# Kernel tuning notes

Measured on AMD Instinct MI355X. Metric: run time of the kernel, lower is better.

## Reference

```python
import jax, jax.numpy as jnp
import numpy as np
from jax import lax

B, S, H = 2, 1024, 1024   # batch, seq, hidden_size
I = 512                   # moe_intermediate_size
E = 16                    # num_experts
TOP_K = 8                 # num_experts_per_tok


def setup_inputs() -> dict:
    key = jax.random.key(0)
    ks = jax.random.split(key, 5)
    scale_h = 1.0 / np.sqrt(H)
    scale_i = 1.0 / np.sqrt(I)
    return {
        "hidden_states": jax.random.normal(ks[0], (B, S, H), dtype=jnp.float32),
        "gate_w": jax.random.normal(ks[1], (H, E), dtype=jnp.float32) * scale_h,   # router
        "w_gate": jax.random.normal(ks[2], (E, H, I), dtype=jnp.float32) * scale_h,
        "w_up":   jax.random.normal(ks[3], (E, H, I), dtype=jnp.float32) * scale_h,
        "w_down": jax.random.normal(ks[4], (E, I, H), dtype=jnp.float32) * scale_i,
    }


def reference(hidden_states, gate_w, w_gate, w_up, w_down):
    b, s, h = hidden_states.shape
    x = hidden_states.reshape(-1, h)                      # [T, H]
    T = x.shape[0]

    router_logits = x @ gate_w                            # [T, E]
    probs = jax.nn.softmax(router_logits.astype(jnp.float32), axis=-1)
    top_w, top_i = lax.top_k(probs, TOP_K)                # [T, K]
    top_w = top_w / jnp.sum(top_w, axis=-1, keepdims=True)  # norm_topk_prob
    top_w = top_w.astype(x.dtype)

    # Dense per-token combine weights [T, E]; zero for unselected experts
    combine = jnp.zeros((T, E), dtype=x.dtype)
    combine = combine.at[jnp.arange(T)[:, None], top_i].add(top_w)

    # Scan over experts: masked gated-MLP, weighted accumulate (exact math;
    # unselected tokens contribute with weight 0, matching index_add scatter).
    def expert_step(acc, ws):
        wg, wu, wd, ce = ws                               # ce: [T] combine weights
        hmid = jax.nn.silu(x @ wg) * (x @ wu)             # [T, I]
        return acc + (hmid @ wd) * ce[:, None], None

    out, _ = lax.scan(expert_step, jnp.zeros_like(x),
                      (w_gate, w_up, w_down, combine.T))
    return out.reshape(b, s, h), router_logits
```

## Files before the change

kernel.cpp:

```cpp
#include <hip/hip_runtime.h>

typedef __attribute__((ext_vector_type(8))) short bf16x8;
typedef __attribute__((ext_vector_type(4))) float f32x4;
typedef __attribute__((ext_vector_type(4))) unsigned short u16x4;


static __device__ __forceinline__ unsigned short f2bfu(float f) {
  union { float f; unsigned u; } v; v.f = f;
  return (unsigned short)((v.u + 0x7fffu + ((v.u >> 16) & 1u)) >> 16);
}

static __device__ __forceinline__ float bfu2f(unsigned short u) {
  union { unsigned u; float f; } v; v.u = ((unsigned)u) << 16; return v.f;
}

static __device__ __forceinline__ void gload_lds16(const void* g, void* l) {
  __builtin_amdgcn_global_load_lds(
      (const __attribute__((address_space(1))) unsigned int*)g,
      (__attribute__((address_space(3))) unsigned int*)l, 16, 0, 0);
}

__global__ __launch_bounds__(256) void k_prep(const float* __restrict__ wga,
                                              const float* __restrict__ wup,
                                              const float* __restrict__ wdo,
                                              unsigned short* __restrict__ wgt,
                                              unsigned short* __restrict__ wut,
                                              unsigned short* __restrict__ wdt2,
                                              const float* __restrict__ x,
                                              const float* __restrict__ gw,
                                              float* __restrict__ combine,
                                              float* __restrict__ logits,
                                              unsigned short* __restrict__ xb) {
  const int bid = blockIdx.x;
  if (bid < 6144) {
    __shared__ float tile[64][65];
    const int zz = bid >> 7;
    const int rem = bid & 127;
    const float* src;
    unsigned short* dst;
    int C, ostride, c0, r0;
    if (zz < 16)      { src = wga + (size_t)zz * 524288; dst = wgt + (size_t)zz * 524288; C = 512; ostride = 1024; c0 = (rem & 7) * 64; r0 = (rem >> 3) * 64; }
    else if (zz < 32) { src = wup + (size_t)(zz-16) * 524288; dst = wut + (size_t)(zz-16) * 524288; C = 512; ostride = 1024; c0 = (rem & 7) * 64; r0 = (rem >> 3) * 64; }
    else              { src = wdo + (size_t)(zz-32) * 524288; dst = wdt2 + (size_t)(zz-32) * 524288; C = 1024; ostride = 512; c0 = (rem & 15) * 64; r0 = (rem >> 4) * 64; }
    int cc = (threadIdx.x & 15) * 4, rr = threadIdx.x >> 4;
#pragma unroll
    for (int i = 0; i < 4; ++i) {
      float4 v = *(const float4*)(src + (size_t)(r0 + rr + i * 16) * C + c0 + cc);
      tile[rr + i * 16][cc + 0] = v.x; tile[rr + i * 16][cc + 1] = v.y;
      tile[rr + i * 16][cc + 2] = v.z; tile[rr + i * 16][cc + 3] = v.w;
    }
    __syncthreads();
#pragma unroll
    for (int i = 0; i < 4; ++i) {
      int oc = rr + i * 16;
      u16x4 o = { f2bfu(tile[cc + 0][oc]), f2bfu(tile[cc + 1][oc]),
                  f2bfu(tile[cc + 2][oc]), f2bfu(tile[cc + 3][oc]) };
      *(u16x4*)(dst + (size_t)(c0 + oc) * ostride + r0 + cc) = o;
    }
    return;
  }
  const int t = (bid - 6144) * 4 + (threadIdx.x >> 6);
  const int lane = threadIdx.x & 63;
  const float* xr = x + (size_t)t * 1024;
  unsigned short* xbr = xb + (size_t)t * 1024;
  float acc[16];
#pragma unroll
  for (int e = 0; e < 16; ++e) acc[e] = 0.f;
  for (int h = lane; h < 1024; h += 64) {
    float xv = xr[h];
    xbr[h] = f2bfu(xv);
    const float4* gr = (const float4*)(gw + (size_t)h * 16);
#pragma unroll
    for (int q = 0; q < 4; ++q) {
      float4 g4 = gr[q];
      acc[q * 4 + 0] += xv * g4.x;
      acc[q * 4 + 1] += xv * g4.y;
      acc[q * 4 + 2] += xv * g4.z;
      acc[q * 4 + 3] += xv * g4.w;
    }
  }
#pragma unroll
  for (int e = 0; e < 16; ++e) {
#pragma unroll
    for (int off = 32; off > 0; off >>= 1)
      acc[e] += __shfl_xor(acc[e], off);
  }
  if (lane < 16) logits[(size_t)t * 16 + lane] = acc[lane];

  float m = acc[0];
#pragma unroll
  for (int e = 1; e < 16; ++e) m = fmaxf(m, acc[e]);
  unsigned sel = 0u;
  for (int k = 0; k < 8; ++k) {
    float best = -3.4e38f; int bi = 0;
#pragma unroll
    for (int e = 0; e < 16; ++e)
      if (!((sel >> e) & 1u) && acc[e] > best) { best = acc[e]; bi = e; }
    sel |= 1u << bi;
  }
  float s = 0.f;
#pragma unroll
  for (int e = 0; e < 16; ++e)
    if ((sel >> e) & 1u) s += expf(acc[e] - m);
  float inv = 1.f / s;
  if (lane < 16)
    combine[(size_t)t * 16 + lane] = ((sel >> lane) & 1u) ? expf(acc[lane] - m) * inv : 0.f;
}

__global__ __launch_bounds__(256) void k_scan(const float* __restrict__ combine,
                                              unsigned short* __restrict__ idxlist,
                                              int* __restrict__ tokslot,
                                              int* __restrict__ counts) {
  __shared__ int wsum[4];
  const int e = blockIdx.x;
  const int tid = threadIdx.x;
  const int lane = tid & 63, w = tid >> 6;
  const int t0 = tid * 8;
  int flags = 0, cnt = 0;
#pragma unroll
  for (int j = 0; j < 8; ++j) {
    float c = combine[(size_t)(t0 + j) * 16 + e];
    if (c != 0.f) { flags |= 1 << j; ++cnt; }
  }
  int scan = cnt;
#pragma unroll
  for (int off = 1; off < 64; off <<= 1) {
    int v = __shfl_up(scan, off);
    if (lane >= off) scan += v;
  }
  if (lane == 63) wsum[w] = scan;
  __syncthreads();
  int base = 0;
  for (int i = 0; i < w; ++i) base += wsum[i];
  int pos = base + scan - cnt;
  for (int j = 0; j < 8; ++j) {
    if ((flags >> j) & 1) {
      idxlist[e * 2048 + pos] = (unsigned short)(t0 + j);
      tokslot[(t0 + j) * 16 + e] = pos;
      ++pos;
    } else {
      tokslot[(t0 + j) * 16 + e] = -1;
    }
  }
  if (tid == 255) counts[e] = base + scan;
}

__global__ __launch_bounds__(256) void k_gateup(const unsigned short* __restrict__ xb,
                                                const unsigned short* __restrict__ wgt,
                                                const unsigned short* __restrict__ wut,
                                                const unsigned short* __restrict__ idxlist,
                                                const int* __restrict__ counts,
                                                unsigned short* __restrict__ midp) {
  const int lb = (int)(blockIdx.x & 7) * 256 + (int)(blockIdx.x >> 3);
  const int p = lb & 255, it = lb >> 8;
  int e = -1, mt = 0, Ne = 0, gb = 0, acc = 0;
#pragma unroll
  for (int i = 0; i < 16; ++i) {
    int c = counts[i];
    int nt = (c + 127) >> 7;
    if (e < 0) {
      if (p < acc + nt) { e = i; mt = p - acc; Ne = c; }
      else gb += c;
    }
    acc += nt;
  }
  if (e < 0) return;
  const int m0 = mt * 128;
  const int i0 = it * 64;

  __shared__ alignas(16) char lds[49152];

  const int tid = threadIdx.x;
  const int lane = tid & 63;
  const int w = tid >> 6;
  const int wm = (w >> 1) * 64;
  const int wn = (w & 1) * 32;

  const int crow = lane >> 2;
  const int slog = (lane & 3) ^ ((crow >> 1) & 3);

  const unsigned short* wge = wgt + (size_t)e * (512 * 1024);
  const unsigned short* wue = wut + (size_t)e * (512 * 1024);

  const unsigned short* gsrc[4];
  int loff[4];
#pragma unroll
  for (int q = 0; q < 4; ++q) {
    int c = w * 4 + q;
    loff[q] = c * 1024;
    if (c < 8) {
      int slot = m0 + c * 16 + crow;
      slot = slot < Ne ? slot : Ne - 1;
      gsrc[q] = xb + (size_t)idxlist[e * 2048 + slot] * 1024 + slog * 8;
    } else if (c < 12) {
      gsrc[q] = wge + (size_t)(i0 + (c - 8) * 16 + crow) * 1024 + slog * 8;
    } else {
      gsrc[q] = wue + (size_t)(i0 + (c - 12) * 16 + crow) * 1024 + slog * 8;
    }
  }

  auto stage = [&](int buf, int k0) {
    char* base = lds + buf * 16384;
#pragma unroll
    for (int q = 0; q < 4; ++q)
      gload_lds16(gsrc[q] + k0, base + loff[q]);
  };

  const int r0 = lane & 15;
  const int gp16 = ((lane >> 4) ^ ((r0 >> 1) & 3)) << 4;
  const int aoff  = ((wm + r0) << 6) + gp16;
  const int bgoff = 8192  + ((wn + r0) << 6) + gp16;
  const int buoff = 12288 + ((wn + r0) << 6) + gp16;

  f32x4 accg[4][2], accu[4][2];
#pragma unroll
  for (int fm = 0; fm < 4; ++fm)
#pragma unroll
    for (int fn = 0; fn < 2; ++fn) {
      accg[fm][fn] = f32x4{0.f, 0.f, 0.f, 0.f};
      accu[fm][fn] = f32x4{0.f, 0.f, 0.f, 0.f};
    }

  stage(0, 0);
  stage(1, 32);
  int cur = 0;
  for (int t = 0; t < 32; ++t) {
    if (t == 31) asm volatile("s_waitcnt vmcnt(0)" ::: "memory");
    else         asm volatile("s_waitcnt vmcnt(4)" ::: "memory");
    __builtin_amdgcn_s_barrier();
    const char* base = lds + cur * 16384;
    bf16x8 a[4], bg[2], bu[2];
#pragma unroll
    for (int fm = 0; fm < 4; ++fm) a[fm] = *(const bf16x8*)(base + aoff + fm * 1024);
#pragma unroll
    for (int fn = 0; fn < 2; ++fn) {
      bg[fn] = *(const bf16x8*)(base + bgoff + fn * 1024);
      bu[fn] = *(const bf16x8*)(base + buoff + fn * 1024);
    }
    asm volatile("s_waitcnt lgkmcnt(0)" ::: "memory");
    __builtin_amdgcn_sched_barrier(0);
    if (t + 2 < 32) {
      int nb = cur + 2; if (nb >= 3) nb -= 3;
      stage(nb, (t + 2) * 32);
    }
    __builtin_amdgcn_s_setprio(1);
#pragma unroll
    for (int fm = 0; fm < 4; ++fm)
#pragma unroll
      for (int fn = 0; fn < 2; ++fn) {
        accg[fm][fn] = __builtin_amdgcn_mfma_f32_16x16x32_bf16(a[fm], bg[fn], accg[fm][fn], 0, 0, 0);
        accu[fm][fn] = __builtin_amdgcn_mfma_f32_16x16x32_bf16(a[fm], bu[fn], accu[fm][fn], 0, 0, 0);
      }
    __builtin_amdgcn_s_setprio(0);
    if (++cur == 3) cur = 0;
  }

  const int gq = lane >> 4;
#pragma unroll
  for (int fm = 0; fm < 4; ++fm) {
#pragma unroll
    for (int jj = 0; jj < 4; ++jj) {
      int slot = m0 + wm + fm * 16 + gq * 4 + jj;
      if (slot >= Ne) continue;
#pragma unroll
      for (int fn = 0; fn < 2; ++fn) {
        float gv = accg[fm][fn][jj];
        float uv = accu[fm][fn][jj];
        float mv = gv / (1.f + __expf(-gv)) * uv;
        midp[(size_t)(gb + slot) * 512 + i0 + wn + fn * 16 + r0] = f2bfu(mv);
      }
    }
  }
}

__global__ __launch_bounds__(512) void k_down(const unsigned short* __restrict__ midp,
                                              const unsigned short* __restrict__ wdt2,
                                              const int* __restrict__ counts,
                                              unsigned short* __restrict__ dpk) {
  const int lb = (int)(blockIdx.x & 7) * 256 + (int)(blockIdx.x >> 3);
  const int mt = lb & 7, ht = (lb >> 3) & 15, e = lb >> 7;
  int Ne = counts[e], gb = 0;
#pragma unroll
  for (int i = 0; i < 16; ++i) { int c = counts[i]; if (i < e) gb += c; }
  const int m0 = mt * 256;
  if (m0 >= Ne) return;
  const int h0 = ht * 64;

  __shared__ alignas(16) char lds[61440];

  const int tid = threadIdx.x;
  const int lane = tid & 63;
  const int w = tid >> 6;
  const int wm = (w >> 1) * 64;
  const int wn = (w & 1) * 32;

  const int crow = lane >> 2;
  const int slog = (lane & 3) ^ ((crow >> 1) & 3);

  const unsigned short* bsrc = wdt2 + (size_t)e * (512 * 1024);

  const unsigned short* gsrcA[2];
  int loffA[2];
#pragma unroll
  for (int q = 0; q < 2; ++q) {
    int c = q * 8 + w;
    loffA[q] = c * 1024;
    int slot = m0 + c * 16 + crow;
    slot = slot < Ne ? slot : Ne - 1;
    gsrcA[q] = midp + (size_t)(gb + slot) * 512 + slog * 8;
  }
  const unsigned short* gsrcB = nullptr;
  int loffB = 0;
  if (w >= 4) {
    loffB = 16384 + (w - 4) * 1024;
    gsrcB = bsrc + (size_t)(h0 + (w - 4) * 16 + crow) * 512 + slog * 8;
  }

  auto stage = [&](int buf, int k0) {
    char* base = lds + buf * 20480;
#pragma unroll
    for (int q = 0; q < 2; ++q)
      gload_lds16(gsrcA[q] + k0, base + loffA[q]);
    if (gsrcB) gload_lds16(gsrcB + k0, base + loffB);
  };

  const int r0 = lane & 15;
  const int gp16 = ((lane >> 4) ^ ((r0 >> 1) & 3)) << 4;
  const int aoff = ((wm + r0) << 6) + gp16;
  const int boff = 16384 + ((wn + r0) << 6) + gp16;

  f32x4 acc[4][2];
#pragma unroll
  for (int fm = 0; fm < 4; ++fm)
#pragma unroll
    for (int fn = 0; fn < 2; ++fn) acc[fm][fn] = f32x4{0.f, 0.f, 0.f, 0.f};

  stage(0, 0);
  stage(1, 32);
  int cur = 0;
  for (int t = 0; t < 16; ++t) {
    if (t == 15)       asm volatile("s_waitcnt vmcnt(0)" ::: "memory");
    else if (w >= 4)   asm volatile("s_waitcnt vmcnt(3)" ::: "memory");
    else               asm volatile("s_waitcnt vmcnt(2)" ::: "memory");
    __builtin_amdgcn_s_barrier();
    const char* base = lds + cur * 20480;
    bf16x8 a[4], b[2];
#pragma unroll
    for (int fm = 0; fm < 4; ++fm) a[fm] = *(const bf16x8*)(base + aoff + fm * 1024);
#pragma unroll
    for (int fn = 0; fn < 2; ++fn) b[fn] = *(const bf16x8*)(base + boff + fn * 1024);
    asm volatile("s_waitcnt lgkmcnt(0)" ::: "memory");
    __builtin_amdgcn_sched_barrier(0);
    if (t + 2 < 16) {
      int nb = cur + 2; if (nb >= 3) nb -= 3;
      stage(nb, (t + 2) * 32);
    }
    __builtin_amdgcn_s_setprio(1);
#pragma unroll
    for (int fm = 0; fm < 4; ++fm)
#pragma unroll
      for (int fn = 0; fn < 2; ++fn)
        acc[fm][fn] = __builtin_amdgcn_mfma_f32_16x16x32_bf16(a[fm], b[fn], acc[fm][fn], 0, 0, 0);
    __builtin_amdgcn_s_setprio(0);
    if (++cur == 3) cur = 0;
  }

  const int gq = lane >> 4;
#pragma unroll
  for (int fm = 0; fm < 4; ++fm)
#pragma unroll
    for (int jj = 0; jj < 4; ++jj) {
      int slot = m0 + wm + fm * 16 + gq * 4 + jj;
      if (slot >= Ne) continue;
#pragma unroll
      for (int fn = 0; fn < 2; ++fn)
        dpk[(size_t)(gb + slot) * 1024 + h0 + wn + fn * 16 + r0] = f2bfu(acc[fm][fn][jj]);
    }
}

__global__ __launch_bounds__(128) void k_combine(const unsigned short* __restrict__ dpk,
                                                 const int* __restrict__ tokslot,
                                                 const int* __restrict__ counts,
                                                 const float* __restrict__ combine,
                                                 float* __restrict__ out) {
  __shared__ int gsl[16];
  __shared__ float cws[16];
  const int t = blockIdx.x;
  const int tid = threadIdx.x;
  if (tid < 16) {
    int eb = 0;
    for (int i = 0; i < tid; ++i) eb += counts[i];
    int sl = tokslot[t * 16 + tid];
    gsl[tid] = (sl >= 0) ? eb + sl : -1;
    cws[tid] = combine[(size_t)t * 16 + tid];
  }
  __syncthreads();
  float av[8];
#pragma unroll
  for (int j = 0; j < 8; ++j) av[j] = 0.f;
#pragma unroll
  for (int e = 0; e < 16; ++e) {
    int g = gsl[e];
    if (g < 0) continue;
    float cw = cws[e];
    bf16x8 v = *(const bf16x8*)(dpk + (size_t)g * 1024 + tid * 8);
#pragma unroll
    for (int j = 0; j < 8; ++j) av[j] += cw * bfu2f((unsigned short)v[j]);
  }
  float4 lo = { av[0], av[1], av[2], av[3] };
  float4 hi = { av[4], av[5], av[6], av[7] };
  float4* op = (float4*)(out + (size_t)t * 1024 + tid * 8);
  op[0] = lo;
  op[1] = hi;
}

extern "C" void kernel_launch(void* const* d_in, const int* in_sizes, int n_in,
                              void* d_out, int out_size, void* d_ws, size_t ws_size,
                              hipStream_t stream) {
  const float* x   = (const float*)d_in[0];
  const float* gw  = (const float*)d_in[1];
  const float* wga = (const float*)d_in[2];
  const float* wup = (const float*)d_in[3];
  const float* wdo = (const float*)d_in[4];
  float* out = (float*)d_out;
  float* logits = out + (size_t)2048 * 1024;

  char* ws = (char*)d_ws;
  unsigned short* xb   = (unsigned short*)(ws + 0);
  unsigned short* wgt  = (unsigned short*)(ws + 4194304);
  unsigned short* wut  = (unsigned short*)(ws + 20971520);
  unsigned short* wdt2 = (unsigned short*)(ws + 37748736);
  unsigned short* midp = (unsigned short*)(ws + 54525952);
  float* combine       = (float*)(ws + 71303168);
  int* tokslot         = (int*)(ws + 71434240);
  unsigned short* idxl = (unsigned short*)(ws + 71565312);
  int* counts          = (int*)(ws + 71630848);
  unsigned short* dpk  = (unsigned short*)(ws + 4194304);

  k_prep<<<6656, 256, 0, stream>>>(wga, wup, wdo, wgt, wut, wdt2, x, gw, combine, logits, xb);
  k_scan<<<16, 256, 0, stream>>>(combine, idxl, tokslot, counts);
  k_gateup<<<2048, 256, 0, stream>>>(xb, wgt, wut, idxl, counts, midp);
  k_down<<<2048, 512, 0, stream>>>(midp, wdt2, counts, dpk);
  k_combine<<<2048, 128, 0, stream>>>(dpk, tokslot, counts, combine, out);
}
```

Before: 143.9 us.

## Fuse gate/up weight fp32-to-bf16 conversion into gateup GEMM loader

Drops the separate transpose-and-convert pass for the gate and up weights in the prep kernel. The gateup kernel now reads the fp32 weights straight from global memory into registers, converts them to bf16, and writes them into LDS. This pipelines the work one stage ahead using double-buffered register arrays and adds a 3-blocks-per-CU launch bound. It removes a 64MB read and 32MB write pass. In exchange each gateup block re-reads fp32 weights, which costs more register pressure and more global traffic across the M tiles.

```diff
diff --git a/kernel.cpp b/kernel.cpp
--- a/kernel.cpp
+++ b/kernel.cpp
@@ -20,11 +20,7 @@
       (__attribute__((address_space(3))) unsigned int*)l, 16, 0, 0);
 }
 
-__global__ __launch_bounds__(256) void k_prep(const float* __restrict__ wga,
-                                              const float* __restrict__ wup,
-                                              const float* __restrict__ wdo,
-                                              unsigned short* __restrict__ wgt,
-                                              unsigned short* __restrict__ wut,
+__global__ __launch_bounds__(256) void k_prep(const float* __restrict__ wdo,
                                               unsigned short* __restrict__ wdt2,
                                               const float* __restrict__ x,
                                               const float* __restrict__ gw,
@@ -32,20 +28,17 @@
                                               float* __restrict__ logits,
                                               unsigned short* __restrict__ xb) {
   const int bid = blockIdx.x;
-  if (bid < 6144) {
+  if (bid < 2048) {
     __shared__ float tile[64][65];
     const int zz = bid >> 7;
     const int rem = bid & 127;
-    const float* src;
-    unsigned short* dst;
-    int C, ostride, c0, r0;
-    if (zz < 16)      { src = wga + (size_t)zz * 524288; dst = wgt + (size_t)zz * 524288; C = 512; ostride = 1024; c0 = (rem & 7) * 64; r0 = (rem >> 3) * 64; }
-    else if (zz < 32) { src = wup + (size_t)(zz-16) * 524288; dst = wut + (size_t)(zz-16) * 524288; C = 512; ostride = 1024; c0 = (rem & 7) * 64; r0 = (rem >> 3) * 64; }
-    else              { src = wdo + (size_t)(zz-32) * 524288; dst = wdt2 + (size_t)(zz-32) * 524288; C = 1024; ostride = 512; c0 = (rem & 15) * 64; r0 = (rem >> 4) * 64; }
+    const float* src = wdo + (size_t)zz * 524288;
+    unsigned short* dst = wdt2 + (size_t)zz * 524288;
+    const int c0 = (rem & 15) * 64, r0 = (rem >> 4) * 64;
     int cc = (threadIdx.x & 15) * 4, rr = threadIdx.x >> 4;
 #pragma unroll
     for (int i = 0; i < 4; ++i) {
-      float4 v = *(const float4*)(src + (size_t)(r0 + rr + i * 16) * C + c0 + cc);
+      float4 v = *(const float4*)(src + (size_t)(r0 + rr + i * 16) * 1024 + c0 + cc);
       tile[rr + i * 16][cc + 0] = v.x; tile[rr + i * 16][cc + 1] = v.y;
       tile[rr + i * 16][cc + 2] = v.z; tile[rr + i * 16][cc + 3] = v.w;
     }
@@ -55,11 +48,11 @@
       int oc = rr + i * 16;
       u16x4 o = { f2bfu(tile[cc + 0][oc]), f2bfu(tile[cc + 1][oc]),
                   f2bfu(tile[cc + 2][oc]), f2bfu(tile[cc + 3][oc]) };
-      *(u16x4*)(dst + (size_t)(c0 + oc) * ostride + r0 + cc) = o;
+      *(u16x4*)(dst + (size_t)(c0 + oc) * 512 + r0 + cc) = o;
     }
     return;
   }
-  const int t = (bid - 6144) * 4 + (threadIdx.x >> 6);
+  const int t = (bid - 2048) * 4 + (threadIdx.x >> 6);
   const int lane = threadIdx.x & 63;
   const float* xr = x + (size_t)t * 1024;
   unsigned short* xbr = xb + (size_t)t * 1024;
@@ -145,12 +138,12 @@
   if (tid == 255) counts[e] = base + scan;
 }
 
-__global__ __launch_bounds__(256) void k_gateup(const unsigned short* __restrict__ xb,
-                                                const unsigned short* __restrict__ wgt,
-                                                const unsigned short* __restrict__ wut,
-                                                const unsigned short* __restrict__ idxlist,
-                                                const int* __restrict__ counts,
-                                                unsigned short* __restrict__ midp) {
+__global__ __launch_bounds__(256, 3) void k_gateup(const unsigned short* __restrict__ xb,
+                                                   const float* __restrict__ wga,
+                                                   const float* __restrict__ wup,
+                                                   const unsigned short* __restrict__ idxlist,
+                                                   const int* __restrict__ counts,
+                                                   unsigned short* __restrict__ midp) {
   const int lb = (int)(blockIdx.x & 7) * 256 + (int)(blockIdx.x >> 3);
   const int p = lb & 255, it = lb >> 8;
   int e = -1, mt = 0, Ne = 0, gb = 0, acc = 0;
@@ -179,31 +172,50 @@
   const int crow = lane >> 2;
   const int slog = (lane & 3) ^ ((crow >> 1) & 3);
 
-  const unsigned short* wge = wgt + (size_t)e * (512 * 1024);
-  const unsigned short* wue = wut + (size_t)e * (512 * 1024);
-
-  const unsigned short* gsrc[4];
-  int loff[4];
-#pragma unroll
-  for (int q = 0; q < 4; ++q) {
-    int c = w * 4 + q;
-    loff[q] = c * 1024;
-    if (c < 8) {
-      int slot = m0 + c * 16 + crow;
-      slot = slot < Ne ? slot : Ne - 1;
-      gsrc[q] = xb + (size_t)idxlist[e * 2048 + slot] * 1024 + slog * 8;
-    } else if (c < 12) {
-      gsrc[q] = wge + (size_t)(i0 + (c - 8) * 16 + crow) * 1024 + slog * 8;
-    } else {
-      gsrc[q] = wue + (size_t)(i0 + (c - 12) * 16 + crow) * 1024 + slog * 8;
-    }
-  }
-
-  auto stage = [&](int buf, int k0) {
+  const float* wge = wga + (size_t)e * 524288;
+  const float* wue = wup + (size_t)e * 524288;
+
+  const unsigned short* gsrcA[2];
+  int loffA[2];
+#pragma unroll
+  for (int q = 0; q < 2; ++q) {
+    int c = w * 2 + q;
+    loffA[q] = c * 1024;
+    int slot = m0 + c * 16 + crow;
+    slot = slot < Ne ? slot : Ne - 1;
+    gsrcA[q] = xb + (size_t)idxlist[e * 2048 + slot] * 1024 + slog * 8;
+  }
+  auto stageA = [&](int buf, int k0) {
     char* base = lds + buf * 16384;
 #pragma unroll
-    for (int q = 0; q < 4; ++q)
-      gload_lds16(gsrc[q] + k0, base + loff[q]);
+    for (int q = 0; q < 2; ++q)
+      gload_lds16(gsrcA[q] + k0, base + loffA[q]);
+  };
+
+  const int iloc = lane;
+  const float* gB = wge + (size_t)(w * 8) * 512 + i0 + iloc;
+  const float* uB = wue + (size_t)(w * 8) * 512 + i0 + iloc;
+  const int bwo = iloc * 64 + ((w ^ ((iloc >> 1) & 3)) << 4);
+
+  auto loadB = [&](float* bv, int T) {
+    const float* g = gB + (size_t)T * 32 * 512;
+    const float* u = uB + (size_t)T * 32 * 512;
+#pragma unroll
+    for (int j = 0; j < 8; ++j) {
+      bv[j] = g[(size_t)j * 512];
+      bv[8 + j] = u[(size_t)j * 512];
+    }
+  };
+  auto cvtwrite = [&](const float* bv, int buf) {
+    bf16x8 pg, pu;
+#pragma unroll
+    for (int j = 0; j < 8; ++j) {
+      pg[j] = (short)f2bfu(bv[j]);
+      pu[j] = (short)f2bfu(bv[8 + j]);
+    }
+    char* base = lds + buf * 16384;
+    *(bf16x8*)(base + 8192 + bwo) = pg;
+    *(bf16x8*)(base + 12288 + bwo) = pu;
   };
 
   const int r0 = lane & 15;
@@ -221,12 +233,17 @@
       accu[fm][fn] = f32x4{0.f, 0.f, 0.f, 0.f};
     }
 
-  stage(0, 0);
-  stage(1, 32);
+  float bvA[16], bvB[16];
+  stageA(0, 0);
+  stageA(1, 32);
+  loadB(bvA, 0);
+  cvtwrite(bvA, 0);
+  loadB(bvB, 1);
+
   int cur = 0;
-  for (int t = 0; t < 32; ++t) {
-    if (t == 31) asm volatile("s_waitcnt vmcnt(0)" ::: "memory");
-    else         asm volatile("s_waitcnt vmcnt(4)" ::: "memory");
+  auto body = [&](int t, float* bvLoad, float* bvCvt) {
+    if (t == 31) asm volatile("s_waitcnt vmcnt(0) lgkmcnt(0)" ::: "memory");
+    else         asm volatile("s_waitcnt vmcnt(18) lgkmcnt(0)" ::: "memory");
     __builtin_amdgcn_s_barrier();
     const char* base = lds + cur * 16384;
     bf16x8 a[4], bg[2], bu[2];
@@ -239,10 +256,13 @@
     }
     asm volatile("s_waitcnt lgkmcnt(0)" ::: "memory");
     __builtin_amdgcn_sched_barrier(0);
+    int nb1 = cur + 1; if (nb1 >= 3) nb1 -= 3;
+    int nb2 = cur + 2; if (nb2 >= 3) nb2 -= 3;
     if (t + 2 < 32) {
-      int nb = cur + 2; if (nb >= 3) nb -= 3;
-      stage(nb, (t + 2) * 32);
-    }
+      loadB(bvLoad, t + 2);
+      stageA(nb2, (t + 2) * 32);
+    }
+    if (t + 1 < 32) cvtwrite(bvCvt, nb1);
     __builtin_amdgcn_s_setprio(1);
 #pragma unroll
     for (int fm = 0; fm < 4; ++fm)
@@ -252,7 +272,12 @@
         accu[fm][fn] = __builtin_amdgcn_mfma_f32_16x16x32_bf16(a[fm], bu[fn], accu[fm][fn], 0, 0, 0);
       }
     __builtin_amdgcn_s_setprio(0);
-    if (++cur == 3) cur = 0;
+    cur = nb1;
+  };
+
+  for (int tt = 0; tt < 16; ++tt) {
+    body(2 * tt, bvA, bvB);
+    body(2 * tt + 1, bvB, bvA);
   }
 
   const int gq = lane >> 4;
@@ -427,19 +452,17 @@
 
   char* ws = (char*)d_ws;
   unsigned short* xb   = (unsigned short*)(ws + 0);
-  unsigned short* wgt  = (unsigned short*)(ws + 4194304);
-  unsigned short* wut  = (unsigned short*)(ws + 20971520);
-  unsigned short* wdt2 = (unsigned short*)(ws + 37748736);
-  unsigned short* midp = (unsigned short*)(ws + 54525952);
+  unsigned short* wdt2 = (unsigned short*)(ws + 4194304);
+  unsigned short* midp = (unsigned short*)(ws + 20971520);
+  unsigned short* dpk  = (unsigned short*)(ws + 37748736);
   float* combine       = (float*)(ws + 71303168);
   int* tokslot         = (int*)(ws + 71434240);
   unsigned short* idxl = (unsigned short*)(ws + 71565312);
   int* counts          = (int*)(ws + 71630848);
-  unsigned short* dpk  = (unsigned short*)(ws + 4194304);
-
-  k_prep<<<6656, 256, 0, stream>>>(wga, wup, wdo, wgt, wut, wdt2, x, gw, combine, logits, xb);
+
+  k_prep<<<2560, 256, 0, stream>>>(wdo, wdt2, x, gw, combine, logits, xb);
   k_scan<<<16, 256, 0, stream>>>(combine, idxl, tokslot, counts);
-  k_gateup<<<2048, 256, 0, stream>>>(xb, wgt, wut, idxl, counts, midp);
+  k_gateup<<<2048, 256, 0, stream>>>(xb, wga, wup, idxl, counts, midp);
   k_down<<<2048, 512, 0, stream>>>(midp, wdt2, counts, dpk);
   k_combine<<<2048, 128, 0, stream>>>(dpk, tokslot, counts, combine, out);
 }
```

After: 145.3 us. Within noise of the previous version (+1.0%).

## Make gate-up and down expert GEMMs persistent with atomic tile scheduling

Applied to the files above, without the earlier changes.

Converts k_gateup and k_down into persistent kernels with smaller fixed grids. Each block repeatedly grabs a work index from a global atomic counter, which k_scan resets, until all valid expert tiles are done. This removes launching many blocks that only exit because their expert has few tokens, balances uneven expert loads dynamically, and orders tiles so consecutive indices share the same token tile. It also adds occupancy hints to the launch bounds. The cost is an atomic plus a block barrier per tile, and a fixed grid size that may not fill the GPU evenly.

```diff
diff --git a/kernel.cpp b/kernel.cpp
--- a/kernel.cpp
+++ b/kernel.cpp
@@ -110,10 +110,12 @@
 __global__ __launch_bounds__(256) void k_scan(const float* __restrict__ combine,
                                               unsigned short* __restrict__ idxlist,
                                               int* __restrict__ tokslot,
-                                              int* __restrict__ counts) {
+                                              int* __restrict__ counts,
+                                              int* __restrict__ ctrs) {
   __shared__ int wsum[4];
   const int e = blockIdx.x;
   const int tid = threadIdx.x;
+  if (e == 0 && tid < 2) ctrs[tid] = 0;
   const int lane = tid & 63, w = tid >> 6;
   const int t0 = tid * 8;
   int flags = 0, cnt = 0;
@@ -145,30 +147,15 @@
   if (tid == 255) counts[e] = base + scan;
 }
 
-__global__ __launch_bounds__(256) void k_gateup(const unsigned short* __restrict__ xb,
-                                                const unsigned short* __restrict__ wgt,
-                                                const unsigned short* __restrict__ wut,
-                                                const unsigned short* __restrict__ idxlist,
-                                                const int* __restrict__ counts,
-                                                unsigned short* __restrict__ midp) {
-  const int lb = (int)(blockIdx.x & 7) * 256 + (int)(blockIdx.x >> 3);
-  const int p = lb & 255, it = lb >> 8;
-  int e = -1, mt = 0, Ne = 0, gb = 0, acc = 0;
-#pragma unroll
-  for (int i = 0; i < 16; ++i) {
-    int c = counts[i];
-    int nt = (c + 127) >> 7;
-    if (e < 0) {
-      if (p < acc + nt) { e = i; mt = p - acc; Ne = c; }
-      else gb += c;
-    }
-    acc += nt;
-  }
-  if (e < 0) return;
-  const int m0 = mt * 128;
-  const int i0 = it * 64;
-
+__global__ __launch_bounds__(256, 3) void k_gateup(const unsigned short* __restrict__ xb,
+                                                   const unsigned short* __restrict__ wgt,
+                                                   const unsigned short* __restrict__ wut,
+                                                   const unsigned short* __restrict__ idxlist,
+                                                   const int* __restrict__ counts,
+                                                   int* __restrict__ ctr,
+                                                   unsigned short* __restrict__ midp) {
   __shared__ alignas(16) char lds[49152];
+  __shared__ int sidx;
 
   const int tid = threadIdx.x;
   const int lane = tid & 63;
@@ -179,114 +166,136 @@
   const int crow = lane >> 2;
   const int slog = (lane & 3) ^ ((crow >> 1) & 3);
 
-  const unsigned short* wge = wgt + (size_t)e * (512 * 1024);
-  const unsigned short* wue = wut + (size_t)e * (512 * 1024);
-
-  const unsigned short* gsrc[4];
-  int loff[4];
-#pragma unroll
-  for (int q = 0; q < 4; ++q) {
-    int c = w * 4 + q;
-    loff[q] = c * 1024;
-    if (c < 8) {
-      int slot = m0 + c * 16 + crow;
-      slot = slot < Ne ? slot : Ne - 1;
-      gsrc[q] = xb + (size_t)idxlist[e * 2048 + slot] * 1024 + slog * 8;
-    } else if (c < 12) {
-      gsrc[q] = wge + (size_t)(i0 + (c - 8) * 16 + crow) * 1024 + slog * 8;
-    } else {
-      gsrc[q] = wue + (size_t)(i0 + (c - 12) * 16 + crow) * 1024 + slog * 8;
-    }
-  }
-
-  auto stage = [&](int buf, int k0) {
-    char* base = lds + buf * 16384;
-#pragma unroll
-    for (int q = 0; q < 4; ++q)
-      gload_lds16(gsrc[q] + k0, base + loff[q]);
-  };
-
   const int r0 = lane & 15;
   const int gp16 = ((lane >> 4) ^ ((r0 >> 1) & 3)) << 4;
   const int aoff  = ((wm + r0) << 6) + gp16;
   const int bgoff = 8192  + ((wn + r0) << 6) + gp16;
   const int buoff = 12288 + ((wn + r0) << 6) + gp16;
-
-  f32x4 accg[4][2], accu[4][2];
-#pragma unroll
-  for (int fm = 0; fm < 4; ++fm)
-#pragma unroll
-    for (int fn = 0; fn < 2; ++fn) {
-      accg[fm][fn] = f32x4{0.f, 0.f, 0.f, 0.f};
-      accu[fm][fn] = f32x4{0.f, 0.f, 0.f, 0.f};
-    }
-
-  stage(0, 0);
-  stage(1, 32);
-  int cur = 0;
-  for (int t = 0; t < 32; ++t) {
-    if (t == 31) asm volatile("s_waitcnt vmcnt(0)" ::: "memory");
-    else         asm volatile("s_waitcnt vmcnt(4)" ::: "memory");
-    __builtin_amdgcn_s_barrier();
-    const char* base = lds + cur * 16384;
-    bf16x8 a[4], bg[2], bu[2];
-#pragma unroll
-    for (int fm = 0; fm < 4; ++fm) a[fm] = *(const bf16x8*)(base + aoff + fm * 1024);
-#pragma unroll
-    for (int fn = 0; fn < 2; ++fn) {
-      bg[fn] = *(const bf16x8*)(base + bgoff + fn * 1024);
-      bu[fn] = *(const bf16x8*)(base + buoff + fn * 1024);
-    }
-    asm volatile("s_waitcnt lgkmcnt(0)" ::: "memory");
-    __builtin_amdgcn_sched_barrier(0);
-    if (t + 2 < 32) {
-      int nb = cur + 2; if (nb >= 3) nb -= 3;
-      stage(nb, (t + 2) * 32);
-    }
-    __builtin_amdgcn_s_setprio(1);
+  const int gq = lane >> 4;
+
+  int cl[16];
+#pragma unroll
+  for (int i = 0; i < 16; ++i) cl[i] = counts[i];
+  int pM = 0;
+#pragma unroll
+  for (int i = 0; i < 16; ++i) pM += (cl[i] + 127) >> 7;
+  const int total = pM * 8;
+
+  while (true) {
+    if (tid == 0) sidx = atomicAdd(ctr, 1);
+    __syncthreads();
+    const int idx = sidx;
+    if (idx >= total) return;
+    const int p = idx >> 3, it = idx & 7;
+    int e = -1, mt = 0, Ne = 0, gb = 0, acc = 0;
+#pragma unroll
+    for (int i = 0; i < 16; ++i) {
+      int c = cl[i];
+      int nt = (c + 127) >> 7;
+      if (e < 0) {
+        if (p < acc + nt) { e = i; mt = p - acc; Ne = c; }
+        else gb += c;
+      }
+      acc += nt;
+    }
+    const int m0 = mt * 128;
+    const int i0 = it * 64;
+
+    const unsigned short* wge = wgt + (size_t)e * (512 * 1024);
+    const unsigned short* wue = wut + (size_t)e * (512 * 1024);
+
+    const unsigned short* gsrc[4];
+    int loff[4];
+#pragma unroll
+    for (int q = 0; q < 4; ++q) {
+      int c = w * 4 + q;
+      loff[q] = c * 1024;
+      if (c < 8) {
+        int slot = m0 + c * 16 + crow;
+        slot = slot < Ne ? slot : Ne - 1;
+        gsrc[q] = xb + (size_t)idxlist[e * 2048 + slot] * 1024 + slog * 8;
+      } else if (c < 12) {
+        gsrc[q] = wge + (size_t)(i0 + (c - 8) * 16 + crow) * 1024 + slog * 8;
+      } else {
+        gsrc[q] = wue + (size_t)(i0 + (c - 12) * 16 + crow) * 1024 + slog * 8;
+      }
+    }
+
+    auto stage = [&](int buf, int k0) {
+      char* base = lds + buf * 16384;
+#pragma unroll
+      for (int q = 0; q < 4; ++q)
+        gload_lds16(gsrc[q] + k0, base + loff[q]);
+    };
+
+    f32x4 accg[4][2], accu[4][2];
 #pragma unroll
     for (int fm = 0; fm < 4; ++fm)
 #pragma unroll
       for (int fn = 0; fn < 2; ++fn) {
-        accg[fm][fn] = __builtin_amdgcn_mfma_f32_16x16x32_bf16(a[fm], bg[fn], accg[fm][fn], 0, 0, 0);
-        accu[fm][fn] = __builtin_amdgcn_mfma_f32_16x16x32_bf16(a[fm], bu[fn], accu[fm][fn], 0, 0, 0);
-      }
-    __builtin_amdgcn_s_setprio(0);
-    if (++cur == 3) cur = 0;
-  }
-
-  const int gq = lane >> 4;
-#pragma unroll
-  for (int fm = 0; fm < 4; ++fm) {
-#pragma unroll
-    for (int jj = 0; jj < 4; ++jj) {
-      int slot = m0 + wm + fm * 16 + gq * 4 + jj;
-      if (slot >= Ne) continue;
+        accg[fm][fn] = f32x4{0.f, 0.f, 0.f, 0.f};
+        accu[fm][fn] = f32x4{0.f, 0.f, 0.f, 0.f};
+      }
+
+    stage(0, 0);
+    stage(1, 32);
+    int cur = 0;
+    for (int t = 0; t < 32; ++t) {
+      if (t == 31) asm volatile("s_waitcnt vmcnt(0)" ::: "memory");
+      else         asm volatile("s_waitcnt vmcnt(4)" ::: "memory");
+      __builtin_amdgcn_s_barrier();
+      const char* base = lds + cur * 16384;
+      bf16x8 a[4], bg[2], bu[2];
+#pragma unroll
+      for (int fm = 0; fm < 4; ++fm) a[fm] = *(const bf16x8*)(base + aoff + fm * 1024);
 #pragma unroll
       for (int fn = 0; fn < 2; ++fn) {
-        float gv = accg[fm][fn][jj];
-        float uv = accu[fm][fn][jj];
-        float mv = gv / (1.f + __expf(-gv)) * uv;
-        midp[(size_t)(gb + slot) * 512 + i0 + wn + fn * 16 + r0] = f2bfu(mv);
-      }
-    }
-  }
-}
-
-__global__ __launch_bounds__(512) void k_down(const unsigned short* __restrict__ midp,
-                                              const unsigned short* __restrict__ wdt2,
-                                              const int* __restrict__ counts,
-                                              unsigned short* __restrict__ dpk) {
-  const int lb = (int)(blockIdx.x & 7) * 256 + (int)(blockIdx.x >> 3);
-  const int mt = lb & 7, ht = (lb >> 3) & 15, e = lb >> 7;
-  int Ne = counts[e], gb = 0;
-#pragma unroll
-  for (int i = 0; i < 16; ++i) { int c = counts[i]; if (i < e) gb += c; }
-  const int m0 = mt * 256;
-  if (m0 >= Ne) return;
-  const int h0 = ht * 64;
-
+        bg[fn] = *(const bf16x8*)(base + bgoff + fn * 1024);
+        bu[fn] = *(const bf16x8*)(base + buoff + fn * 1024);
+      }
+      asm volatile("s_waitcnt lgkmcnt(0)" ::: "memory");
+      __builtin_amdgcn_sched_barrier(0);
+      if (t + 2 < 32) {
+        int nb = cur + 2; if (nb >= 3) nb -= 3;
+        stage(nb, (t + 2) * 32);
+      }
+      __builtin_amdgcn_s_setprio(1);
+#pragma unroll
+      for (int fm = 0; fm < 4; ++fm)
+#pragma unroll
+        for (int fn = 0; fn < 2; ++fn) {
+          accg[fm][fn] = __builtin_amdgcn_mfma_f32_16x16x32_bf16(a[fm], bg[fn], accg[fm][fn], 0, 0, 0);
+          accu[fm][fn] = __builtin_amdgcn_mfma_f32_16x16x32_bf16(a[fm], bu[fn], accu[fm][fn], 0, 0, 0);
+        }
+      __builtin_amdgcn_s_setprio(0);
+      if (++cur == 3) cur = 0;
+    }
+
+#pragma unroll
+    for (int fm = 0; fm < 4; ++fm) {
+#pragma unroll
+      for (int jj = 0; jj < 4; ++jj) {
+        int slot = m0 + wm + fm * 16 + gq * 4 + jj;
+        if (slot >= Ne) continue;
+#pragma unroll
+        for (int fn = 0; fn < 2; ++fn) {
+          float gv = accg[fm][fn][jj];
+          float uv = accu[fm][fn][jj];
+          float mv = gv / (1.f + __expf(-gv)) * uv;
+          midp[(size_t)(gb + slot) * 512 + i0 + wn + fn * 16 + r0] = f2bfu(mv);
+        }
+      }
+    }
+  }
+}
+
+__global__ __launch_bounds__(512, 4) void k_down(const unsigned short* __restrict__ midp,
+                                                 const unsigned short* __restrict__ wdt2,
+                                                 const int* __restrict__ counts,
+                                                 int* __restrict__ ctr,
+                                                 unsigned short* __restrict__ dpk) {
   __shared__ alignas(16) char lds[61440];
+  __shared__ int sidx;
 
   const int tid = threadIdx.x;
   const int lane = tid & 63;
@@ -297,85 +306,114 @@
   const int crow = lane >> 2;
   const int slog = (lane & 3) ^ ((crow >> 1) & 3);
 
-  const unsigned short* bsrc = wdt2 + (size_t)e * (512 * 1024);
-
-  const unsigned short* gsrcA[2];
-  int loffA[2];
-#pragma unroll
-  for (int q = 0; q < 2; ++q) {
-    int c = q * 8 + w;
-    loffA[q] = c * 1024;
-    int slot = m0 + c * 16 + crow;
-    slot = slot < Ne ? slot : Ne - 1;
-    gsrcA[q] = midp + (size_t)(gb + slot) * 512 + slog * 8;
-  }
-  const unsigned short* gsrcB = nullptr;
-  int loffB = 0;
-  if (w >= 4) {
-    loffB = 16384 + (w - 4) * 1024;
-    gsrcB = bsrc + (size_t)(h0 + (w - 4) * 16 + crow) * 512 + slog * 8;
-  }
-
-  auto stage = [&](int buf, int k0) {
-    char* base = lds + buf * 20480;
-#pragma unroll
-    for (int q = 0; q < 2; ++q)
-      gload_lds16(gsrcA[q] + k0, base + loffA[q]);
-    if (gsrcB) gload_lds16(gsrcB + k0, base + loffB);
-  };
-
   const int r0 = lane & 15;
   const int gp16 = ((lane >> 4) ^ ((r0 >> 1) & 3)) << 4;
   const int aoff = ((wm + r0) << 6) + gp16;
   const int boff = 16384 + ((wn + r0) << 6) + gp16;
-
-  f32x4 acc[4][2];
-#pragma unroll
-  for (int fm = 0; fm < 4; ++fm)
-#pragma unroll
-    for (int fn = 0; fn < 2; ++fn) acc[fm][fn] = f32x4{0.f, 0.f, 0.f, 0.f};
-
-  stage(0, 0);
-  stage(1, 32);
-  int cur = 0;
-  for (int t = 0; t < 16; ++t) {
-    if (t == 15)       asm volatile("s_waitcnt vmcnt(0)" ::: "memory");
-    else if (w >= 4)   asm volatile("s_waitcnt vmcnt(3)" ::: "memory");
-    else               asm volatile("s_waitcnt vmcnt(2)" ::: "memory");
-    __builtin_amdgcn_s_barrier();
-    const char* base = lds + cur * 20480;
-    bf16x8 a[4], b[2];
-#pragma unroll
-    for (int fm = 0; fm < 4; ++fm) a[fm] = *(const bf16x8*)(base + aoff + fm * 1024);
-#pragma unroll
-    for (int fn = 0; fn < 2; ++fn) b[fn] = *(const bf16x8*)(base + boff + fn * 1024);
-    asm volatile("s_waitcnt lgkmcnt(0)" ::: "memory");
-    __builtin_amdgcn_sched_barrier(0);
-    if (t + 2 < 16) {
-      int nb = cur + 2; if (nb >= 3) nb -= 3;
-      stage(nb, (t + 2) * 32);
-    }
-    __builtin_amdgcn_s_setprio(1);
+  const int gq = lane >> 4;
+
+  int cl[16];
+#pragma unroll
+  for (int i = 0; i < 16; ++i) cl[i] = counts[i];
+  int pM = 0;
+#pragma unroll
+  for (int i = 0; i < 16; ++i) pM += (cl[i] + 255) >> 8;
+  const int total = pM * 16;
+
+  while (true) {
+    if (tid == 0) sidx = atomicAdd(ctr, 1);
+    __syncthreads();
+    const int idx = sidx;
+    if (idx >= total) return;
+    const int p = idx >> 4, ht = idx & 15;
+    int e = -1, mt = 0, Ne = 0, gb = 0, acc0 = 0;
+#pragma unroll
+    for (int i = 0; i < 16; ++i) {
+      int c = cl[i];
+      int nt = (c + 255) >> 8;
+      if (e < 0) {
+        if (p < acc0 + nt) { e = i; mt = p - acc0; Ne = c; }
+        else gb += c;
+      }
+      acc0 += nt;
+    }
+    const int m0 = mt * 256;
+    const int h0 = ht * 64;
+
+    const unsigned short* bsrc = wdt2 + (size_t)e * (512 * 1024);
+
+    const unsigned short* gsrcA[2];
+    int loffA[2];
+#pragma unroll
+    for (int q = 0; q < 2; ++q) {
+      int c = q * 8 + w;
+      loffA[q] = c * 1024;
+      int slot = m0 + c * 16 + crow;
+      slot = slot < Ne ? slot : Ne - 1;
+      gsrcA[q] = midp + (size_t)(gb + slot) * 512 + slog * 8;
+    }
+    const unsigned short* gsrcB = nullptr;
+    int loffB = 0;
+    if (w >= 4) {
+      loffB = 16384 + (w - 4) * 1024;
+      gsrcB = bsrc + (size_t)(h0 + (w - 4) * 16 + crow) * 512 + slog * 8;
+    }
+
+    auto stage = [&](int buf, int k0) {
+      char* base = lds + buf * 20480;
+#pragma unroll
+      for (int q = 0; q < 2; ++q)
+        gload_lds16(gsrcA[q] + k0, base + loffA[q]);
+      if (gsrcB) gload_lds16(gsrcB + k0, base + loffB);
+    };
+
+    f32x4 acc[4][2];
 #pragma unroll
     for (int fm = 0; fm < 4; ++fm)
 #pragma unroll
-      for (int fn = 0; fn < 2; ++fn)
-        acc[fm][fn] = __builtin_amdgcn_mfma_f32_16x16x32_bf16(a[fm], b[fn], acc[fm][fn], 0, 0, 0);
-    __builtin_amdgcn_s_setprio(0);
-    if (++cur == 3) cur = 0;
-  }
-
-  const int gq = lane >> 4;
-#pragma unroll
-  for (int fm = 0; fm < 4; ++fm)
-#pragma unroll
-    for (int jj = 0; jj < 4; ++jj) {
-      int slot = m0 + wm + fm * 16 + gq * 4 + jj;
-      if (slot >= Ne) continue;
-#pragma unroll
-      for (int fn = 0; fn < 2; ++fn)
-        dpk[(size_t)(gb + slot) * 1024 + h0 + wn + fn * 16 + r0] = f2bfu(acc[fm][fn][jj]);
-    }
+      for (int fn = 0; fn < 2; ++fn) acc[fm][fn] = f32x4{0.f, 0.f, 0.f, 0.f};
+
+    stage(0, 0);
+    stage(1, 32);
+    int cur = 0;
+    for (int t = 0; t < 16; ++t) {
+      if (t == 15)       asm volatile("s_waitcnt vmcnt(0)" ::: "memory");
+      else if (w >= 4)   asm volatile("s_waitcnt vmcnt(3)" ::: "memory");
+      else               asm volatile("s_waitcnt vmcnt(2)" ::: "memory");
+      __builtin_amdgcn_s_barrier();
+      const char* base = lds + cur * 20480;
+      bf16x8 a[4], b[2];
+#pragma unroll
+      for (int fm = 0; fm < 4; ++fm) a[fm] = *(const bf16x8*)(base + aoff + fm * 1024);
+#pragma unroll
+      for (int fn = 0; fn < 2; ++fn) b[fn] = *(const bf16x8*)(base + boff + fn * 1024);
+      asm volatile("s_waitcnt lgkmcnt(0)" ::: "memory");
+      __builtin_amdgcn_sched_barrier(0);
+      if (t + 2 < 16) {
+        int nb = cur + 2; if (nb >= 3) nb -= 3;
+        stage(nb, (t + 2) * 32);
+      }
+      __builtin_amdgcn_s_setprio(1);
+#pragma unroll
+      for (int fm = 0; fm < 4; ++fm)
+#pragma unroll
+        for (int fn = 0; fn < 2; ++fn)
+          acc[fm][fn] = __builtin_amdgcn_mfma_f32_16x16x32_bf16(a[fm], b[fn], acc[fm][fn], 0, 0, 0);
+      __builtin_amdgcn_s_setprio(0);
+      if (++cur == 3) cur = 0;
+    }
+
+#pragma unroll
+    for (int fm = 0; fm < 4; ++fm)
+#pragma unroll
+      for (int jj = 0; jj < 4; ++jj) {
+        int slot = m0 + wm + fm * 16 + gq * 4 + jj;
+        if (slot >= Ne) continue;
+#pragma unroll
+        for (int fn = 0; fn < 2; ++fn)
+          dpk[(size_t)(gb + slot) * 1024 + h0 + wn + fn * 16 + r0] = f2bfu(acc[fm][fn][jj]);
+      }
+  }
 }
 
 __global__ __launch_bounds__(128) void k_combine(const unsigned short* __restrict__ dpk,
@@ -435,11 +473,12 @@
   int* tokslot         = (int*)(ws + 71434240);
   unsigned short* idxl = (unsigned short*)(ws + 71565312);
   int* counts          = (int*)(ws + 71630848);
+  int* ctrs            = (int*)(ws + 71630912);
   unsigned short* dpk  = (unsigned short*)(ws + 4194304);
 
   k_prep<<<6656, 256, 0, stream>>>(wga, wup, wdo, wgt, wut, wdt2, x, gw, combine, logits, xb);
-  k_scan<<<16, 256, 0, stream>>>(combine, idxl, tokslot, counts);
-  k_gateup<<<2048, 256, 0, stream>>>(xb, wgt, wut, idxl, counts, midp);
-  k_down<<<2048, 512, 0, stream>>>(midp, wdt2, counts, dpk);
+  k_scan<<<16, 256, 0, stream>>>(combine, idxl, tokslot, counts, ctrs);
+  k_gateup<<<768, 256, 0, stream>>>(xb, wgt, wut, idxl, counts, ctrs + 0, midp);
+  k_down<<<512, 512, 0, stream>>>(midp, wdt2, counts, ctrs + 1, dpk);
   k_combine<<<2048, 128, 0, stream>>>(dpk, tokslot, counts, combine, out);
 }
```

Measured after the change: 167.3 us. 1.16x slower.
